# Optimization experiments

Measured on AMD Instinct MI355X. Metric: run time of the kernel, lower is better.

## Reference

```python
import jax, jax.numpy as jnp
import numpy as np

EMBED = 1024
HEADS = 16
HEAD_DIM = EMBED // HEADS


def _rope(t):
    # t: (B, S, H, D) -> rotary embedding applied over last dim (GPT-NeoX rotate-half)
    B, S, H, D = t.shape
    half = D // 2
    inv_freq = 1.0 / (10000.0 ** (jnp.arange(0, half, dtype=jnp.float32) / half))
    freqs = jnp.arange(S, dtype=jnp.float32)[:, None] * inv_freq[None, :]  # (S, half)
    cos = jnp.cos(freqs)[None, :, None, :]
    sin = jnp.sin(freqs)[None, :, None, :]
    t1, t2 = t[..., :half], t[..., half:]
    return jnp.concatenate([t1 * cos - t2 * sin, t2 * cos + t1 * sin], axis=-1)


def setup_inputs() -> dict:
    key = jax.random.key(0)
    k1, k2, k3 = jax.random.split(key, 3)
    B, S = 2, 2048
    x = jax.random.normal(k1, (B, S, EMBED), dtype=jnp.float32)
    attn_mask = jnp.ones((B, S), dtype=bool)
    w_qkv = jax.random.normal(k2, (EMBED, 3 * EMBED), dtype=jnp.float32) * (1.0 / np.sqrt(EMBED))
    w_out = jax.random.normal(k3, (EMBED, EMBED), dtype=jnp.float32) * (1.0 / np.sqrt(EMBED))
    return {"x": x, "attn_mask": attn_mask, "w_qkv": w_qkv, "w_out": w_out, "is_causal": 1}


def reference(x, attn_mask, w_qkv, w_out, is_causal):
    B, S, E = x.shape
    qkv = x @ w_qkv                                   # (B, S, 3E)
    q, k, v = jnp.split(qkv, 3, axis=-1)
    q = q.reshape(B, S, HEADS, HEAD_DIM)
    k = k.reshape(B, S, HEADS, HEAD_DIM)
    v = v.reshape(B, S, HEADS, HEAD_DIM)
    q = _rope(q)
    k = _rope(k)
    scale = 1.0 / np.sqrt(HEAD_DIM)
    scores = jnp.einsum('bqhd,bkhd->bhqk', q, k) * scale  # (B, H, S, S)
    neg = jnp.asarray(-1e30, dtype=scores.dtype)
    if is_causal:
        causal = jnp.tril(jnp.ones((S, S), dtype=bool))
        scores = jnp.where(causal[None, None], scores, neg)
    else:
        scores = jnp.where(attn_mask[:, None, None, :], scores, neg)
    attn = jax.nn.softmax(scores, axis=-1)
    y = jnp.einsum('bhqk,bkhd->bqhd', attn, v).reshape(B, S, E)
    return y @ w_out
```

## Files before the change

### kernel.cpp

```cpp
#include <hip/hip_runtime.h>
#include <hip/hip_bf16.h>
#include <stdint.h>

typedef float v4f __attribute__((ext_vector_type(4)));
typedef short v8s __attribute__((ext_vector_type(8)));

#define LOG2E 1.44269504088896f
#define QSCALE (0.125f * LOG2E)
#define SOFTMAX_OFF 16.0f

__device__ __forceinline__ unsigned short f2bf(float f) {
    unsigned int u = __float_as_uint(f);
    u += 0x7fffu + ((u >> 16) & 1u);
    return (unsigned short)(u >> 16);
}

#define LDS_FENCE() __builtin_amdgcn_fence(__ATOMIC_ACQ_REL, "workgroup")

__device__ __forceinline__ void gload_lds16(const unsigned short* g, unsigned short* s) {
    __builtin_amdgcn_global_load_lds(
        (const __attribute__((address_space(1))) unsigned int*)g,
        (__attribute__((address_space(3))) unsigned int*)s, 16, 0, 0);
}

__global__ void k_cast_bf16(const float* __restrict__ src,
                            unsigned short* __restrict__ dst, int n4) {
    int i = blockIdx.x * blockDim.x + threadIdx.x;
    int stride = gridDim.x * blockDim.x;
    for (; i < n4; i += stride) {
        float4 v = ((const float4*)src)[i];
        ushort4 o;
        o.x = f2bf(v.x); o.y = f2bf(v.y); o.z = f2bf(v.z); o.w = f2bf(v.w);
        ((ushort4*)dst)[i] = o;
    }
}

__global__ void k_transpose_both(const float* __restrict__ w_qkv,
                                 const float* __restrict__ w_out,
                                 unsigned short* __restrict__ wqkvT,
                                 unsigned short* __restrict__ woutT) {
    __shared__ unsigned short tile[64][65];
    int id = blockIdx.x;
    const float* src; unsigned short* dst; int N, kb, nb;
    if (id < 768) { src = w_qkv; dst = wqkvT; N = 3072; nb = (id % 48) * 64; kb = (id / 48) * 64; }
    else { id -= 768; src = w_out; dst = woutT; N = 1024; nb = (id % 16) * 64; kb = (id / 16) * 64; }
    const int K = 1024;
    int t = threadIdx.x;
    for (int i = 0; i < 16; ++i) {
        int e = t + i * 256;
        int n_l = e & 63, k_l = e >> 6;
        tile[n_l][k_l] = f2bf(src[(size_t)(kb + k_l) * N + nb + n_l]);
    }
    __syncthreads();
    for (int i = 0; i < 16; ++i) {
        int e = t + i * 256;
        int k_l = e & 63, n_l = e >> 6;
        dst[(size_t)(nb + n_l) * K + kb + k_l] = tile[n_l][k_l];
    }
}

__global__ __launch_bounds__(256) void k_gemm_qkv(
    const unsigned short* __restrict__ A,
    const unsigned short* __restrict__ Bt,
    unsigned short* __restrict__ Qg,
    unsigned short* __restrict__ Kg,
    unsigned short* __restrict__ Vg) {
    const int K = 1024, N = 3072;
    __shared__ __align__(16) unsigned short Ab[128 * 32];
    __shared__ __align__(16) unsigned short Bb[128 * 32];
    const int t = threadIdx.x;
    const int w = t >> 6, l = t & 63, quad = l >> 4, ln = l & 15;
    const int wm = (w >> 1) * 64, wn = (w & 1) * 64;
    const int mb = blockIdx.y * 128, nb = blockIdx.x * 128;

    v4f acc[4][4];
#pragma unroll
    for (int i = 0; i < 4; ++i)
#pragma unroll
        for (int j = 0; j < 4; ++j) acc[i][j] = (v4f){0.f, 0.f, 0.f, 0.f};

    for (int k0 = 0; k0 < K; k0 += 32) {
        __syncthreads();
#pragma unroll
        for (int u = 0; u < 2; ++u) {
            int e = t + u * 256;
            gload_lds16(A + (size_t)(mb + (e >> 2)) * K + k0 + (e & 3) * 8,
                        &Ab[(size_t)(w * 64 + u * 256) * 8]);
            gload_lds16(Bt + (size_t)(nb + (e >> 2)) * K + k0 + (e & 3) * 8,
                        &Bb[(size_t)(w * 64 + u * 256) * 8]);
        }
        __syncthreads();
        v8s af[4], bfr[4];
#pragma unroll
        for (int i = 0; i < 4; ++i)
            af[i] = *(const v8s*)&Ab[(wm + i * 16 + ln) * 32 + quad * 8];
#pragma unroll
        for (int j = 0; j < 4; ++j)
            bfr[j] = *(const v8s*)&Bb[(wn + j * 16 + ln) * 32 + quad * 8];
#pragma unroll
        for (int i = 0; i < 4; ++i)
#pragma unroll
            for (int j = 0; j < 4; ++j)
                acc[i][j] = __builtin_amdgcn_mfma_f32_16x16x32_bf16(
                    af[i], bfr[j], acc[i][j], 0, 0, 0);
    }

    const int col0 = nb + wn;
    const int region = col0 >> 10;
    const int h = (col0 & 1023) >> 6;
    unsigned short* dst = (region == 0) ? Qg : (region == 1) ? Kg : Vg;

    if (region == 2) {
#pragma unroll
        for (int i = 0; i < 4; ++i)
#pragma unroll
            for (int r = 0; r < 4; ++r) {
                int row = mb + wm + i * 16 + quad * 4 + r;
                int s = row & 2047, b = row >> 11;
                size_t base = ((size_t)(b * 16 + h) * 2048 + s) * 64;
#pragma unroll
                for (int j = 0; j < 4; ++j)
                    dst[base + j * 16 + ln] = f2bf(acc[i][j][r]);
            }
    } else {
        const float scale = (region == 0) ? QSCALE : 1.0f;
#pragma unroll
        for (int jj = 0; jj < 2; ++jj) {
            float inv = __expf(-(float)(jj * 16 + ln) * 0.28782313662425572f);
#pragma unroll
            for (int i = 0; i < 4; ++i)
#pragma unroll
                for (int r = 0; r < 4; ++r) {
                    int row = mb + wm + i * 16 + quad * 4 + r;
                    int s = row & 2047, b = row >> 11;
                    float sn, cs;
                    sincosf((float)s * inv, &sn, &cs);
                    float t1 = acc[i][jj][r], t2 = acc[i][jj + 2][r];
                    size_t base = ((size_t)(b * 16 + h) * 2048 + s) * 64;
                    dst[base + jj * 16 + ln]      = f2bf((t1 * cs - t2 * sn) * scale);
                    dst[base + jj * 16 + ln + 32] = f2bf((t2 * cs + t1 * sn) * scale);
                }
        }
    }
}

__global__ void k_vtrans(const unsigned short* __restrict__ Vg,
                         unsigned short* __restrict__ Vt) {
    __shared__ unsigned short vtile[64][65];
    const int bh = blockIdx.y, sb = blockIdx.x * 64;
    const int t = threadIdx.x;
    const unsigned short* src = Vg + (size_t)bh * 2048 * 64;
    for (int i = 0; i < 16; ++i) {
        int e = t + i * 256;
        int d = e & 63, s_l = e >> 6;
        vtile[d][s_l] = src[(size_t)(sb + s_l) * 64 + d];
    }
    __syncthreads();
    for (int i = 0; i < 16; ++i) {
        int e = t + i * 256;
        int s_l = e & 63, d = e >> 6;
        Vt[(size_t)(bh * 64 + d) * 2048 + sb + s_l] = vtile[d][s_l];
    }
}

template<bool BF16OUT>
__global__ __launch_bounds__(256) void k_gemm_bt(
    const unsigned short* __restrict__ A,
    const unsigned short* __restrict__ Bt,
    void* __restrict__ Cv, int M, int N, int K) {
    __shared__ __align__(16) unsigned short Ab[128 * 32];
    __shared__ __align__(16) unsigned short Bb[128 * 32];
    const int t = threadIdx.x;
    const int w = t >> 6, l = t & 63, quad = l >> 4, ln = l & 15;
    const int wm = (w >> 1) * 64, wn = (w & 1) * 64;
    const int mb = blockIdx.y * 128, nb = blockIdx.x * 128;

    v4f acc[4][4];
#pragma unroll
    for (int i = 0; i < 4; ++i)
#pragma unroll
        for (int j = 0; j < 4; ++j) acc[i][j] = (v4f){0.f, 0.f, 0.f, 0.f};

    for (int k0 = 0; k0 < K; k0 += 32) {
        __syncthreads();
#pragma unroll
        for (int u = 0; u < 2; ++u) {
            int e = t + u * 256;
            gload_lds16(A + (size_t)(mb + (e >> 2)) * K + k0 + (e & 3) * 8,
                        &Ab[(size_t)(w * 64 + u * 256) * 8]);
            gload_lds16(Bt + (size_t)(nb + (e >> 2)) * K + k0 + (e & 3) * 8,
                        &Bb[(size_t)(w * 64 + u * 256) * 8]);
        }
        __syncthreads();
        v8s af[4], bfr[4];
#pragma unroll
        for (int i = 0; i < 4; ++i)
            af[i] = *(const v8s*)&Ab[(wm + i * 16 + ln) * 32 + quad * 8];
#pragma unroll
        for (int j = 0; j < 4; ++j)
            bfr[j] = *(const v8s*)&Bb[(wn + j * 16 + ln) * 32 + quad * 8];
#pragma unroll
        for (int i = 0; i < 4; ++i)
#pragma unroll
            for (int j = 0; j < 4; ++j)
                acc[i][j] = __builtin_amdgcn_mfma_f32_16x16x32_bf16(
                    af[i], bfr[j], acc[i][j], 0, 0, 0);
    }

#pragma unroll
    for (int i = 0; i < 4; ++i) {
        int r0 = mb + wm + i * 16 + quad * 4;
#pragma unroll
        for (int j = 0; j < 4; ++j) {
            int c0 = nb + wn + j * 16 + ln;
#pragma unroll
            for (int r = 0; r < 4; ++r) {
                if (BF16OUT)
                    ((unsigned short*)Cv)[(size_t)(r0 + r) * N + c0] = f2bf(acc[i][j][r]);
                else
                    ((float*)Cv)[(size_t)(r0 + r) * N + c0] = acc[i][j][r];
            }
        }
    }
}

__global__ __launch_bounds__(256) void k_flash(
    const unsigned short* __restrict__ Qg,
    const unsigned short* __restrict__ Kg,
    const unsigned short* __restrict__ Vt,
    unsigned short* __restrict__ Og) {
    __shared__ __align__(16) unsigned short Kb[2][64 * 64];
    __shared__ __align__(16) unsigned short Vb[2][64 * 64];
    __shared__ __align__(16) unsigned short P[4][16][72];

    const int id = blockIdx.x;
    const int xcd = id & 7, slot = id >> 3;
    const int bh = xcd * 4 + (slot & 3);
    const int qt = 31 - (slot >> 2);
    const int qbase = qt * 64;
    const int nit = qt + 1;

    const int t = threadIdx.x, w = t >> 6, l = t & 63, quad = l >> 4, ln = l & 15;
    const int b = bh >> 4, h = bh & 15;

    const unsigned short* Qp = Qg + (size_t)bh * 2048 * 64;
    const unsigned short* Kp = Kg + (size_t)bh * 2048 * 64;
    const unsigned short* Vp = Vt + (size_t)bh * 64 * 2048;

    unsigned kst[2], vst[2];
    int cchunk = l & 7, rloc = l >> 3;
#pragma unroll
    for (int j = 0; j < 2; ++j) {
        int c = w + j * 4;
        int rr = c * 8 + rloc;
        int g = (cchunk + rr) & 7;
        kst[j] = (unsigned)(rr * 64 + g * 8);
        vst[j] = (unsigned)(rr * 2048 + g * 8);
    }
    const int c0 = ((quad - ln) & 7) * 8;
    const int c1 = ((quad + 4 - ln) & 7) * 8;
    const v8s ones = {0x3F80, 0x3F80, 0x3F80, 0x3F80, 0x3F80, 0x3F80, 0x3F80, 0x3F80};

    const int qrow = qbase + w * 16 + ln;
    v8s qf0 = *(const v8s*)(Qp + (size_t)qrow * 64 + quad * 8);
    v8s qf1 = *(const v8s*)(Qp + (size_t)qrow * 64 + quad * 8 + 32);

    v4f oacc[5];
#pragma unroll
    for (int dt = 0; dt < 5; ++dt) oacc[dt] = (v4f){0.f, 0.f, 0.f, 0.f};

    auto stage = [&](int buf, int kvb) {
        const unsigned short* kg = Kp + (size_t)kvb * 64;
        const unsigned short* vg = Vp + kvb;
#pragma unroll
        for (int j = 0; j < 2; ++j) {
            int c = w + j * 4;
            gload_lds16(kg + kst[j], &Kb[buf][c * 512]);
            gload_lds16(vg + vst[j], &Vb[buf][c * 512]);
        }
    };

    auto compute = [&](int buf, int it) {
        v4f sc[4];
#pragma unroll
        for (int kt = 0; kt < 4; ++kt) {
            int row = kt * 16 + ln;
            v8s k0 = *(const v8s*)&Kb[buf][row * 64 + c0];
            v8s k1 = *(const v8s*)&Kb[buf][row * 64 + c1];
            sc[kt] = (v4f){0.f, 0.f, 0.f, 0.f};
            sc[kt] = __builtin_amdgcn_mfma_f32_16x16x32_bf16(qf0, k0, sc[kt], 0, 0, 0);
            sc[kt] = __builtin_amdgcn_mfma_f32_16x16x32_bf16(qf1, k1, sc[kt], 0, 0, 0);
        }
        if (it == qt) {
            int q0 = qbase + w * 16 + quad * 4;
#pragma unroll
            for (int kt = 0; kt < 4; ++kt) {
                int kv = qbase + kt * 16 + ln;
#pragma unroll
                for (int r = 0; r < 4; ++r)
                    if (kv > q0 + r) sc[kt][r] = -1e30f;
            }
        }
#pragma unroll
        for (int kt = 0; kt < 4; ++kt)
#pragma unroll
            for (int r = 0; r < 4; ++r)
                sc[kt][r] = exp2f(sc[kt][r] - SOFTMAX_OFF);

#pragma unroll
        for (int kt = 0; kt < 4; ++kt) {
            union { __hip_bfloat162 hh; unsigned int u; } p01, p23;
            p01.hh = __float22bfloat162_rn(make_float2(sc[kt][0], sc[kt][1]));
            p23.hh = __float22bfloat162_rn(make_float2(sc[kt][2], sc[kt][3]));
            P[w][quad * 4 + 0][kt * 16 + ln] = (unsigned short)p01.u;
            P[w][quad * 4 + 1][kt * 16 + ln] = (unsigned short)(p01.u >> 16);
            P[w][quad * 4 + 2][kt * 16 + ln] = (unsigned short)p23.u;
            P[w][quad * 4 + 3][kt * 16 + ln] = (unsigned short)(p23.u >> 16);
        }
        LDS_FENCE();
        v8s pf0 = *(const v8s*)&P[w][ln][quad * 8];
        v8s pf1 = *(const v8s*)&P[w][ln][quad * 8 + 32];
        LDS_FENCE();
#pragma unroll
        for (int dt = 0; dt < 4; ++dt) {
            int row = dt * 16 + ln;
            v8s v0 = *(const v8s*)&Vb[buf][row * 64 + c0];
            v8s v1 = *(const v8s*)&Vb[buf][row * 64 + c1];
            oacc[dt] = __builtin_amdgcn_mfma_f32_16x16x32_bf16(pf0, v0, oacc[dt], 0, 0, 0);
            oacc[dt] = __builtin_amdgcn_mfma_f32_16x16x32_bf16(pf1, v1, oacc[dt], 0, 0, 0);
        }
        oacc[4] = __builtin_amdgcn_mfma_f32_16x16x32_bf16(pf0, ones, oacc[4], 0, 0, 0);
        oacc[4] = __builtin_amdgcn_mfma_f32_16x16x32_bf16(pf1, ones, oacc[4], 0, 0, 0);
    };

    stage(0, 0);
    int it = 0;
    for (;;) {
        __syncthreads();
        stage(1, (it + 1) * 64);
        compute(0, it);
        if (++it >= nit) break;
        __syncthreads();
        stage(0, (it + 1) * 64);
        compute(1, it);
        if (++it >= nit) break;
    }

    float rden[4];
#pragma unroll
    for (int r = 0; r < 4; ++r) rden[r] = 1.f / oacc[4][r];
#pragma unroll
    for (int dt = 0; dt < 4; ++dt)
#pragma unroll
        for (int r = 0; r < 4; ++r) {
            int s = qbase + w * 16 + quad * 4 + r;
            Og[(size_t)(b * 2048 + s) * 1024 + h * 64 + dt * 16 + ln] =
                f2bf(oacc[dt][r] * rden[r]);
        }
}

extern "C" void kernel_launch(void* const* d_in, const int* in_sizes, int n_in,
                              void* d_out, int out_size, void* d_ws, size_t ws_size,
                              hipStream_t stream) {
    const float* x     = (const float*)d_in[0];
    const float* w_qkv = (const float*)d_in[2];
    const float* w_out = (const float*)d_in[3];
    char* ws = (char*)d_ws;

    unsigned short* xb    = (unsigned short*)(ws);
    unsigned short* wqkvT = (unsigned short*)(ws + (size_t)(8 << 20));
    unsigned short* woutT = (unsigned short*)(ws + (size_t)(14 << 20));
    unsigned short* Qg    = (unsigned short*)(ws + (size_t)(16 << 20));
    unsigned short* Kg    = (unsigned short*)(ws + (size_t)(24 << 20));
    unsigned short* Vg    = (unsigned short*)(ws + (size_t)(32 << 20));
    unsigned short* Vt    = (unsigned short*)(ws + (size_t)(40 << 20));
    unsigned short* Og    = (unsigned short*)(ws + (size_t)(48 << 20));

    k_cast_bf16<<<1024, 256, 0, stream>>>(x, xb, 4096 * 1024 / 4);
    k_transpose_both<<<1024, 256, 0, stream>>>(w_qkv, w_out, wqkvT, woutT);
    k_gemm_qkv<<<dim3(24, 32), 256, 0, stream>>>(xb, wqkvT, Qg, Kg, Vg);
    k_vtrans<<<dim3(32, 32), 256, 0, stream>>>(Vg, Vt);
    k_flash<<<1024, 256, 0, stream>>>(Qg, Kg, Vt, Og);
    k_gemm_bt<false><<<dim3(8, 32), 256, 0, stream>>>(Og, woutT, (float*)d_out, 4096, 1024, 1024);
}
```

Before: 214.3 us.

## Merge prep kernels, fuse V transpose into QKV GEMM, double-buffer GEMMs, tabulate RoPE

The x cast and weight transposes now run in one prep kernel, which also fills a cos/sin RoPE table so the QKV GEMM epilogue no longer calls sincosf per element. The QKV GEMM writes V already transposed through an LDS staging tile, which removes the separate V-transpose kernel and the round trip through global memory. Both GEMMs double-buffer their LDS tiles so the next K-slice load overlaps the current MFMAs, at the cost of one barrier per step and twice the shared memory. Together these cut two kernel launches and some global traffic.

```diff
diff --git a/kernel.cpp b/kernel.cpp
--- a/kernel.cpp
+++ b/kernel.cpp
@@ -23,29 +23,42 @@
         (__attribute__((address_space(3))) unsigned int*)s, 16, 0, 0);
 }
 
-__global__ void k_cast_bf16(const float* __restrict__ src,
-                            unsigned short* __restrict__ dst, int n4) {
-    int i = blockIdx.x * blockDim.x + threadIdx.x;
-    int stride = gridDim.x * blockDim.x;
-    for (; i < n4; i += stride) {
-        float4 v = ((const float4*)src)[i];
-        ushort4 o;
-        o.x = f2bf(v.x); o.y = f2bf(v.y); o.z = f2bf(v.z); o.w = f2bf(v.w);
-        ((ushort4*)dst)[i] = o;
-    }
-}
-
-__global__ void k_transpose_both(const float* __restrict__ w_qkv,
-                                 const float* __restrict__ w_out,
-                                 unsigned short* __restrict__ wqkvT,
-                                 unsigned short* __restrict__ woutT) {
+__global__ void k_prep(const float* __restrict__ x,
+                       const float* __restrict__ w_qkv,
+                       const float* __restrict__ w_out,
+                       unsigned short* __restrict__ xb,
+                       unsigned short* __restrict__ wqkvT,
+                       unsigned short* __restrict__ woutT,
+                       float2* __restrict__ rope) {
     __shared__ unsigned short tile[64][65];
-    int id = blockIdx.x;
+    int id = blockIdx.x, t = threadIdx.x;
+    if (id < 1024) {
+        int base = id * 256 + t;
+#pragma unroll
+        for (int k = 0; k < 4; ++k) {
+            int i = base + k * 262144;
+            float4 v = ((const float4*)x)[i];
+            ushort4 o;
+            o.x = f2bf(v.x); o.y = f2bf(v.y); o.z = f2bf(v.z); o.w = f2bf(v.w);
+            ((ushort4*)xb)[i] = o;
+        }
+        return;
+    }
+    id -= 1024;
+    if (id < 256) {
+        int idx = id * 256 + t;
+        int s = idx >> 5, d = idx & 31;
+        float inv = __expf(-(float)d * 0.28782313662425572f);
+        float sn, cs;
+        sincosf((float)s * inv, &sn, &cs);
+        rope[idx] = make_float2(cs, sn);
+        return;
+    }
+    id -= 256;
     const float* src; unsigned short* dst; int N, kb, nb;
     if (id < 768) { src = w_qkv; dst = wqkvT; N = 3072; nb = (id % 48) * 64; kb = (id / 48) * 64; }
     else { id -= 768; src = w_out; dst = woutT; N = 1024; nb = (id % 16) * 64; kb = (id / 16) * 64; }
     const int K = 1024;
-    int t = threadIdx.x;
     for (int i = 0; i < 16; ++i) {
         int e = t + i * 256;
         int n_l = e & 63, k_l = e >> 6;
@@ -62,12 +75,15 @@
 __global__ __launch_bounds__(256) void k_gemm_qkv(
     const unsigned short* __restrict__ A,
     const unsigned short* __restrict__ Bt,
+    const float2* __restrict__ rope,
     unsigned short* __restrict__ Qg,
     unsigned short* __restrict__ Kg,
-    unsigned short* __restrict__ Vg) {
-    const int K = 1024, N = 3072;
-    __shared__ __align__(16) unsigned short Ab[128 * 32];
-    __shared__ __align__(16) unsigned short Bb[128 * 32];
+    unsigned short* __restrict__ Vt) {
+    const int K = 1024;
+    __shared__ __align__(16) union {
+        struct { unsigned short Ab[2][4096], Bb[2][4096]; } g;
+        unsigned short vt[2][64][136];
+    } sm;
     const int t = threadIdx.x;
     const int w = t >> 6, l = t & 63, quad = l >> 4, ln = l & 15;
     const int wm = (w >> 1) * 64, wn = (w & 1) * 64;
@@ -79,97 +95,92 @@
 #pragma unroll
         for (int j = 0; j < 4; ++j) acc[i][j] = (v4f){0.f, 0.f, 0.f, 0.f};
 
-    for (int k0 = 0; k0 < K; k0 += 32) {
-        __syncthreads();
+    auto stage = [&](int buf, int k0) {
 #pragma unroll
         for (int u = 0; u < 2; ++u) {
             int e = t + u * 256;
             gload_lds16(A + (size_t)(mb + (e >> 2)) * K + k0 + (e & 3) * 8,
-                        &Ab[(size_t)(w * 64 + u * 256) * 8]);
+                        &sm.g.Ab[buf][(w * 64 + u * 256) * 8]);
             gload_lds16(Bt + (size_t)(nb + (e >> 2)) * K + k0 + (e & 3) * 8,
-                        &Bb[(size_t)(w * 64 + u * 256) * 8]);
-        }
-        __syncthreads();
+                        &sm.g.Bb[buf][(w * 64 + u * 256) * 8]);
+        }
+    };
+
+    stage(0, 0);
+    int buf = 0;
+    for (int itk = 0; itk < 32; ++itk) {
+        __syncthreads();
+        if (itk + 1 < 32) stage(buf ^ 1, (itk + 1) * 32);
         v8s af[4], bfr[4];
 #pragma unroll
         for (int i = 0; i < 4; ++i)
-            af[i] = *(const v8s*)&Ab[(wm + i * 16 + ln) * 32 + quad * 8];
+            af[i] = *(const v8s*)&sm.g.Ab[buf][(wm + i * 16 + ln) * 32 + quad * 8];
 #pragma unroll
         for (int j = 0; j < 4; ++j)
-            bfr[j] = *(const v8s*)&Bb[(wn + j * 16 + ln) * 32 + quad * 8];
+            bfr[j] = *(const v8s*)&sm.g.Bb[buf][(wn + j * 16 + ln) * 32 + quad * 8];
 #pragma unroll
         for (int i = 0; i < 4; ++i)
 #pragma unroll
             for (int j = 0; j < 4; ++j)
                 acc[i][j] = __builtin_amdgcn_mfma_f32_16x16x32_bf16(
                     af[i], bfr[j], acc[i][j], 0, 0, 0);
-    }
-
-    const int col0 = nb + wn;
-    const int region = col0 >> 10;
-    const int h = (col0 & 1023) >> 6;
-    unsigned short* dst = (region == 0) ? Qg : (region == 1) ? Kg : Vg;
-
-    if (region == 2) {
+        buf ^= 1;
+    }
+
+    if (nb >= 2048) {
+        __syncthreads();
+        const int hh = wn >> 6;
+#pragma unroll
+        for (int i = 0; i < 4; ++i)
+#pragma unroll
+            for (int j = 0; j < 4; ++j) {
+                int d = j * 16 + ln;
+#pragma unroll
+                for (int r = 0; r < 4; ++r)
+                    sm.vt[hh][d][wm + i * 16 + quad * 4 + r] = f2bf(acc[i][j][r]);
+            }
+        __syncthreads();
+        const int hbase = (nb & 1023) >> 6;
+        const int b = mb >> 11, sbase = mb & 2047;
+#pragma unroll
+        for (int i = 0; i < 8; ++i) {
+            int c = t + i * 256;
+            int h2 = c >> 10, dd = (c >> 4) & 63, off = (c & 15) * 8;
+            v8s val = *(const v8s*)&sm.vt[h2][dd][off];
+            *(v8s*)(Vt + ((size_t)((b * 16 + hbase + h2) * 64 + dd) * 2048 + sbase + off)) = val;
+        }
+        return;
+    }
+
+    const int region = (nb + wn) >> 10;
+    const int h = ((nb + wn) & 1023) >> 6;
+    unsigned short* dst = region == 0 ? Qg : Kg;
+    const float scale = region == 0 ? QSCALE : 1.0f;
+#pragma unroll
+    for (int jj = 0; jj < 2; ++jj) {
+        const float2* rp = rope + jj * 16 + ln;
 #pragma unroll
         for (int i = 0; i < 4; ++i)
 #pragma unroll
             for (int r = 0; r < 4; ++r) {
                 int row = mb + wm + i * 16 + quad * 4 + r;
                 int s = row & 2047, b = row >> 11;
+                float2 cs = rp[s * 32];
+                float t1 = acc[i][jj][r], t2 = acc[i][jj + 2][r];
                 size_t base = ((size_t)(b * 16 + h) * 2048 + s) * 64;
-#pragma unroll
-                for (int j = 0; j < 4; ++j)
-                    dst[base + j * 16 + ln] = f2bf(acc[i][j][r]);
+                dst[base + jj * 16 + ln]      = f2bf((t1 * cs.x - t2 * cs.y) * scale);
+                dst[base + jj * 16 + ln + 32] = f2bf((t2 * cs.x + t1 * cs.y) * scale);
             }
-    } else {
-        const float scale = (region == 0) ? QSCALE : 1.0f;
-#pragma unroll
-        for (int jj = 0; jj < 2; ++jj) {
-            float inv = __expf(-(float)(jj * 16 + ln) * 0.28782313662425572f);
-#pragma unroll
-            for (int i = 0; i < 4; ++i)
-#pragma unroll
-                for (int r = 0; r < 4; ++r) {
-                    int row = mb + wm + i * 16 + quad * 4 + r;
-                    int s = row & 2047, b = row >> 11;
-                    float sn, cs;
-                    sincosf((float)s * inv, &sn, &cs);
-                    float t1 = acc[i][jj][r], t2 = acc[i][jj + 2][r];
-                    size_t base = ((size_t)(b * 16 + h) * 2048 + s) * 64;
-                    dst[base + jj * 16 + ln]      = f2bf((t1 * cs - t2 * sn) * scale);
-                    dst[base + jj * 16 + ln + 32] = f2bf((t2 * cs + t1 * sn) * scale);
-                }
-        }
-    }
-}
-
-__global__ void k_vtrans(const unsigned short* __restrict__ Vg,
-                         unsigned short* __restrict__ Vt) {
-    __shared__ unsigned short vtile[64][65];
-    const int bh = blockIdx.y, sb = blockIdx.x * 64;
-    const int t = threadIdx.x;
-    const unsigned short* src = Vg + (size_t)bh * 2048 * 64;
-    for (int i = 0; i < 16; ++i) {
-        int e = t + i * 256;
-        int d = e & 63, s_l = e >> 6;
-        vtile[d][s_l] = src[(size_t)(sb + s_l) * 64 + d];
-    }
-    __syncthreads();
-    for (int i = 0; i < 16; ++i) {
-        int e = t + i * 256;
-        int s_l = e & 63, d = e >> 6;
-        Vt[(size_t)(bh * 64 + d) * 2048 + sb + s_l] = vtile[d][s_l];
-    }
-}
-
-template<bool BF16OUT>
-__global__ __launch_bounds__(256) void k_gemm_bt(
+    }
+}
+
+__global__ __launch_bounds__(256) void k_gemm_out(
     const unsigned short* __restrict__ A,
     const unsigned short* __restrict__ Bt,
-    void* __restrict__ Cv, int M, int N, int K) {
-    __shared__ __align__(16) unsigned short Ab[128 * 32];
-    __shared__ __align__(16) unsigned short Bb[128 * 32];
+    float* __restrict__ C) {
+    const int K = 1024, N = 1024;
+    __shared__ __align__(16) unsigned short Ab[2][4096];
+    __shared__ __align__(16) unsigned short Bb[2][4096];
     const int t = threadIdx.x;
     const int w = t >> 6, l = t & 63, quad = l >> 4, ln = l & 15;
     const int wm = (w >> 1) * 64, wn = (w & 1) * 64;
@@ -181,30 +192,36 @@
 #pragma unroll
         for (int j = 0; j < 4; ++j) acc[i][j] = (v4f){0.f, 0.f, 0.f, 0.f};
 
-    for (int k0 = 0; k0 < K; k0 += 32) {
-        __syncthreads();
+    auto stage = [&](int buf, int k0) {
 #pragma unroll
         for (int u = 0; u < 2; ++u) {
             int e = t + u * 256;
             gload_lds16(A + (size_t)(mb + (e >> 2)) * K + k0 + (e & 3) * 8,
-                        &Ab[(size_t)(w * 64 + u * 256) * 8]);
+                        &Ab[buf][(w * 64 + u * 256) * 8]);
             gload_lds16(Bt + (size_t)(nb + (e >> 2)) * K + k0 + (e & 3) * 8,
-                        &Bb[(size_t)(w * 64 + u * 256) * 8]);
-        }
-        __syncthreads();
+                        &Bb[buf][(w * 64 + u * 256) * 8]);
+        }
+    };
+
+    stage(0, 0);
+    int buf = 0;
+    for (int itk = 0; itk < 32; ++itk) {
+        __syncthreads();
+        if (itk + 1 < 32) stage(buf ^ 1, (itk + 1) * 32);
         v8s af[4], bfr[4];
 #pragma unroll
         for (int i = 0; i < 4; ++i)
-            af[i] = *(const v8s*)&Ab[(wm + i * 16 + ln) * 32 + quad * 8];
+            af[i] = *(const v8s*)&Ab[buf][(wm + i * 16 + ln) * 32 + quad * 8];
 #pragma unroll
         for (int j = 0; j < 4; ++j)
-            bfr[j] = *(const v8s*)&Bb[(wn + j * 16 + ln) * 32 + quad * 8];
+            bfr[j] = *(const v8s*)&Bb[buf][(wn + j * 16 + ln) * 32 + quad * 8];
 #pragma unroll
         for (int i = 0; i < 4; ++i)
 #pragma unroll
             for (int j = 0; j < 4; ++j)
                 acc[i][j] = __builtin_amdgcn_mfma_f32_16x16x32_bf16(
                     af[i], bfr[j], acc[i][j], 0, 0, 0);
+        buf ^= 1;
     }
 
 #pragma unroll
@@ -214,12 +231,8 @@
         for (int j = 0; j < 4; ++j) {
             int c0 = nb + wn + j * 16 + ln;
 #pragma unroll
-            for (int r = 0; r < 4; ++r) {
-                if (BF16OUT)
-                    ((unsigned short*)Cv)[(size_t)(r0 + r) * N + c0] = f2bf(acc[i][j][r]);
-                else
-                    ((float*)Cv)[(size_t)(r0 + r) * N + c0] = acc[i][j][r];
-            }
+            for (int r = 0; r < 4; ++r)
+                C[(size_t)(r0 + r) * N + c0] = acc[i][j][r];
         }
     }
 }
@@ -372,14 +385,12 @@
     unsigned short* woutT = (unsigned short*)(ws + (size_t)(14 << 20));
     unsigned short* Qg    = (unsigned short*)(ws + (size_t)(16 << 20));
     unsigned short* Kg    = (unsigned short*)(ws + (size_t)(24 << 20));
-    unsigned short* Vg    = (unsigned short*)(ws + (size_t)(32 << 20));
-    unsigned short* Vt    = (unsigned short*)(ws + (size_t)(40 << 20));
-    unsigned short* Og    = (unsigned short*)(ws + (size_t)(48 << 20));
-
-    k_cast_bf16<<<1024, 256, 0, stream>>>(x, xb, 4096 * 1024 / 4);
-    k_transpose_both<<<1024, 256, 0, stream>>>(w_qkv, w_out, wqkvT, woutT);
-    k_gemm_qkv<<<dim3(24, 32), 256, 0, stream>>>(xb, wqkvT, Qg, Kg, Vg);
-    k_vtrans<<<dim3(32, 32), 256, 0, stream>>>(Vg, Vt);
+    unsigned short* Vt    = (unsigned short*)(ws + (size_t)(32 << 20));
+    unsigned short* Og    = (unsigned short*)(ws + (size_t)(40 << 20));
+    float2*         rope  = (float2*)(ws + (size_t)(48 << 20));
+
+    k_prep<<<2304, 256, 0, stream>>>(x, w_qkv, w_out, xb, wqkvT, woutT, rope);
+    k_gemm_qkv<<<dim3(24, 32), 256, 0, stream>>>(xb, wqkvT, rope, Qg, Kg, Vt);
     k_flash<<<1024, 256, 0, stream>>>(Qg, Kg, Vt, Og);
-    k_gemm_bt<false><<<dim3(8, 32), 256, 0, stream>>>(Og, woutT, (float*)d_out, 4096, 1024, 1024);
-}
+    k_gemm_out<<<dim3(8, 32), 256, 0, stream>>>(Og, woutT, (float*)d_out);
+}
```

Measured after the change: 196.7 us. 1.09x faster.
